# Optimization experiments

Hardware: AMD Instinct MI355X
Metric: run time of the kernel (lower is better)

Reference implementation:

```python
import jax, jax.numpy as jnp
import numpy as np

N_NODES = 50000
N_EDGES = 800000
N_GRAPHS = 1024
NODE_IN = 128
HID = 300
DEPTH = 5
READOUT = 1024


def setup_inputs() -> dict:
    key = jax.random.key(0)
    ks = jax.random.split(key, 12)
    x = jax.random.normal(ks[0], (N_NODES, NODE_IN), dtype=jnp.float32)
    edge_index = jax.random.randint(ks[1], (2, N_EDGES), 0, N_NODES, dtype=jnp.int32)
    batch = jnp.sort(jax.random.randint(ks[2], (N_NODES,), 0, N_GRAPHS, dtype=jnp.int32))
    s_in = 1.0 / np.sqrt(NODE_IN)
    s_h = 1.0 / np.sqrt(HID)
    W_proj = jax.random.normal(ks[3], (NODE_IN, HID), dtype=jnp.float32) * s_in
    b_proj = jnp.zeros((HID,), dtype=jnp.float32)
    W1 = jax.random.normal(ks[4], (DEPTH, HID, HID), dtype=jnp.float32) * s_h
    b1 = jnp.zeros((DEPTH, HID), dtype=jnp.float32)
    W2 = jax.random.normal(ks[5], (DEPTH, HID, HID), dtype=jnp.float32) * s_h
    b2 = jnp.zeros((DEPTH, HID), dtype=jnp.float32)
    W_sp = jax.random.normal(ks[6], (HID, READOUT), dtype=jnp.float32) * s_h
    b_sp = jnp.zeros((READOUT,), dtype=jnp.float32)
    prelu_a = jnp.full((1,), 0.25, dtype=jnp.float32)  # nn.PReLU default
    return {"x": x, "edge_index": edge_index, "batch": batch,
            "W_proj": W_proj, "b_proj": b_proj, "W1": W1, "b1": b1,
            "W2": W2, "b2": b2, "W_sp": W_sp, "b_sp": b_sp, "prelu_a": prelu_a}


def reference(x, edge_index, batch, W_proj, b_proj, W1, b1, W2, b2, W_sp, b_sp, prelu_a):
    # project_node_feats: Linear + ReLU
    h = jax.nn.relu(x @ W_proj + b_proj)  # [N, HID]
    src = edge_index[0]
    dst = edge_index[1]
    for i in range(DEPTH):
        # GINConv (eps=0): out = nn(x + sum_{j in N(i)} x_j)
        agg = h + jax.ops.segment_sum(h[src], dst, num_segments=N_NODES)
        h = jax.nn.relu(agg @ W1[i] + b1[i]) @ W2[i] + b2[i]
        if i < DEPTH - 1:
            h = jax.nn.relu(h)
        # dropout is identity in eval mode
    # global_add_pool over graph ids
    pooled = jax.ops.segment_sum(h, batch, num_segments=N_GRAPHS)  # [G, HID]
    z = pooled @ W_sp + b_sp  # [G, READOUT]
    # PReLU with single shared parameter
    readout = jnp.where(z >= 0, z, prelu_a[0] * z)
    return readout
```

## Files before the change

kernel.cpp:

```cpp
#include <hip/hip_runtime.h>
#include <cstdint>

#define N_NODES 50000
#define N_EDGES 800000
#define N_GRAPHS 1024
#define NODE_IN 128
#define HID 300
#define DEPTH 5
#define READOUT 1024
#define PSTR 320
#define XSTR 384

typedef float f32x4 __attribute__((ext_vector_type(4)));
typedef short bf16x8 __attribute__((ext_vector_type(8)));
typedef unsigned short us8 __attribute__((ext_vector_type(8)));

__device__ inline unsigned short f2bf(float v) {
    unsigned u = __float_as_uint(v);
    unsigned r = u + 0x7FFFu + ((u >> 16) & 1u);
    return (unsigned short)(r >> 16);
}
__device__ inline float bf2f(unsigned short h) {
    return __uint_as_float((unsigned)h << 16);
}
__device__ inline float bflo(unsigned u) { return __uint_as_float(u << 16); }
__device__ inline float bfhi(unsigned u) { return __uint_as_float(u & 0xFFFF0000u); }
__device__ inline unsigned packbf(float a, float b) {
    return (unsigned)f2bf(a) | ((unsigned)f2bf(b) << 16);
}

__global__ void hist_kernel(const int* __restrict__ dst, int* __restrict__ cnt, int n) {
    int i = blockIdx.x * blockDim.x + threadIdx.x;
    if (i < n) atomicAdd(&cnt[dst[i]], 1);
}

__global__ __launch_bounds__(256)
void scan_block(const int* __restrict__ in, int* __restrict__ out_excl,
                int* __restrict__ bsum, int n) {
    __shared__ int buf[256];
    int i = blockIdx.x * 256 + (int)threadIdx.x;
    int v = (i < n) ? in[i] : 0;
    buf[threadIdx.x] = v;
    __syncthreads();
    for (int off = 1; off < 256; off <<= 1) {
        int t = ((int)threadIdx.x >= off) ? buf[threadIdx.x - off] : 0;
        __syncthreads();
        buf[threadIdx.x] += t;
        __syncthreads();
    }
    if (i < n) out_excl[i] = buf[threadIdx.x] - v;
    if (threadIdx.x == 255) bsum[blockIdx.x] = buf[255];
}

__global__ __launch_bounds__(256)
void scan_base(const int* __restrict__ bsum, int* __restrict__ bbase, int nb,
               int* __restrict__ total) {
    __shared__ int buf[256];
    int v = ((int)threadIdx.x < nb) ? bsum[threadIdx.x] : 0;
    buf[threadIdx.x] = v;
    __syncthreads();
    for (int off = 1; off < 256; off <<= 1) {
        int t = ((int)threadIdx.x >= off) ? buf[threadIdx.x - off] : 0;
        __syncthreads();
        buf[threadIdx.x] += t;
        __syncthreads();
    }
    if ((int)threadIdx.x < nb) bbase[threadIdx.x] = buf[threadIdx.x] - v;
    if (threadIdx.x == 255) *total = buf[255];
}

__global__ void scan_add(int* __restrict__ offs, const int* __restrict__ bbase,
                         int* __restrict__ cursor, int n) {
    int i = blockIdx.x * blockDim.x + threadIdx.x;
    if (i < n) {
        int o = offs[i] + bbase[blockIdx.x];
        offs[i] = o;
        cursor[i] = o;
    }
}

__global__ void scatter_kernel(const int* __restrict__ src, const int* __restrict__ dst,
                               int* __restrict__ cursor, int* __restrict__ csr, int n) {
    int i = blockIdx.x * blockDim.x + threadIdx.x;
    if (i < n) {
        int p = atomicAdd(&cursor[dst[i]], 1);
        csr[p] = src[i];
    }
}

__global__ __launch_bounds__(256)
void aggregate_bf16(const unsigned short* __restrict__ h, const int* __restrict__ offs,
                    const int* __restrict__ csr, unsigned short* __restrict__ out) {
    int wave = (int)((blockIdx.x * blockDim.x + threadIdx.x) >> 6);
    int lane = threadIdx.x & 63;
    if (wave >= N_NODES) return;
    float a0, a1, a2, a3, a4, a5;
    {
        const unsigned* r = (const unsigned*)(h + (size_t)wave * PSTR);
        uint2 u = *(const uint2*)&r[2 * lane];
        unsigned t = (lane < 32) ? r[128 + lane] : 0u;
        a0 = bflo(u.x); a1 = bfhi(u.x);
        a2 = bflo(u.y); a3 = bfhi(u.y);
        a4 = bflo(t);   a5 = bfhi(t);
    }
    int s = offs[wave], e = offs[wave + 1];
    int k = s;
    for (; k + 3 < e; k += 4) {
        const unsigned* r0 = (const unsigned*)(h + (size_t)csr[k] * PSTR);
        const unsigned* r1 = (const unsigned*)(h + (size_t)csr[k + 1] * PSTR);
        const unsigned* r2 = (const unsigned*)(h + (size_t)csr[k + 2] * PSTR);
        const unsigned* r3 = (const unsigned*)(h + (size_t)csr[k + 3] * PSTR);
        uint2 x0 = *(const uint2*)&r0[2 * lane];
        uint2 x1 = *(const uint2*)&r1[2 * lane];
        uint2 x2 = *(const uint2*)&r2[2 * lane];
        uint2 x3 = *(const uint2*)&r3[2 * lane];
        unsigned t0 = 0, t1 = 0, t2 = 0, t3 = 0;
        if (lane < 32) {
            t0 = r0[128 + lane]; t1 = r1[128 + lane];
            t2 = r2[128 + lane]; t3 = r3[128 + lane];
        }
        a0 += bflo(x0.x) + bflo(x1.x) + bflo(x2.x) + bflo(x3.x);
        a1 += bfhi(x0.x) + bfhi(x1.x) + bfhi(x2.x) + bfhi(x3.x);
        a2 += bflo(x0.y) + bflo(x1.y) + bflo(x2.y) + bflo(x3.y);
        a3 += bfhi(x0.y) + bfhi(x1.y) + bfhi(x2.y) + bfhi(x3.y);
        a4 += bflo(t0) + bflo(t1) + bflo(t2) + bflo(t3);
        a5 += bfhi(t0) + bfhi(t1) + bfhi(t2) + bfhi(t3);
    }
    for (; k < e; ++k) {
        const unsigned* r = (const unsigned*)(h + (size_t)csr[k] * PSTR);
        uint2 u = *(const uint2*)&r[2 * lane];
        unsigned t = (lane < 32) ? r[128 + lane] : 0u;
        a0 += bflo(u.x); a1 += bfhi(u.x);
        a2 += bflo(u.y); a3 += bfhi(u.y);
        a4 += bflo(t);   a5 += bfhi(t);
    }
    unsigned* o = (unsigned*)(out + (size_t)wave * PSTR);
    uint2 w; w.x = packbf(a0, a1); w.y = packbf(a2, a3);
    *(uint2*)&o[2 * lane] = w;
    if (lane < 32) o[128 + lane] = (lane < 22) ? packbf(a4, a5) : 0u;
}

__global__ __launch_bounds__(256)
void split_weight_t(const float* __restrict__ W, int K, int N, int KP,
                    unsigned short* __restrict__ H, unsigned short* __restrict__ L) {
    __shared__ float tile[32][33];
    int n0 = blockIdx.x * 32, k0 = blockIdx.y * 32;
    int tx = threadIdx.x & 31, ty = threadIdx.x >> 5;
#pragma unroll
    for (int r = 0; r < 4; ++r) {
        int k = k0 + ty + r * 8, n = n0 + tx;
        tile[ty + r * 8][tx] = (k < K && n < N) ? W[(size_t)k * N + n] : 0.f;
    }
    __syncthreads();
#pragma unroll
    for (int r = 0; r < 4; ++r) {
        int n = n0 + ty + r * 8, k = k0 + tx;
        float v = tile[tx][ty + r * 8];
        unsigned short hb = f2bf(v);
        H[(size_t)n * KP + k] = hb;
        L[(size_t)n * KP + k] = f2bf(v - bf2f(hb));
    }
}

__global__ __launch_bounds__(256)
void split_wproj(const float* __restrict__ W, unsigned short* __restrict__ Bp) {
    __shared__ float tile[32][33];
    int n0 = blockIdx.x * 32, k0 = blockIdx.y * 32;
    int tx = threadIdx.x & 31, ty = threadIdx.x >> 5;
#pragma unroll
    for (int r = 0; r < 4; ++r) {
        int k = k0 + ty + r * 8, n = n0 + tx;
        tile[ty + r * 8][tx] = (k < NODE_IN && n < HID) ? W[(size_t)k * HID + n] : 0.f;
    }
    __syncthreads();
#pragma unroll
    for (int r = 0; r < 4; ++r) {
        int n = n0 + ty + r * 8, k = k0 + tx;
        float v = tile[tx][ty + r * 8];
        unsigned short hb = f2bf(v);
        unsigned short lb = f2bf(v - bf2f(hb));
        Bp[(size_t)n * XSTR + k] = hb;
        Bp[(size_t)n * XSTR + 128 + k] = hb;
        Bp[(size_t)n * XSTR + 256 + k] = lb;
    }
}

__global__ void split_x(const float* __restrict__ x, unsigned short* __restrict__ xs) {
    int i = blockIdx.x * blockDim.x + threadIdx.x;
    if (i >= N_NODES * 64) return;
    int row = i >> 6, c = i & 63;
    float2 v = *(const float2*)&x[(size_t)row * NODE_IN + 2 * c];
    unsigned short h0 = f2bf(v.x), h1 = f2bf(v.y);
    unsigned short l0 = f2bf(v.x - bf2f(h0)), l1 = f2bf(v.y - bf2f(h1));
    unsigned hp = (unsigned)h0 | ((unsigned)h1 << 16);
    unsigned lp = (unsigned)l0 | ((unsigned)l1 << 16);
    unsigned* o = (unsigned*)(xs + (size_t)row * XSTR);
    o[c] = hp;
    o[64 + c] = lp;
    o[128 + c] = hp;
}

#define BSWZ(r, c) ((c) ^ (((r) >> 1) & 3))
__global__ __launch_bounds__(512)
void gin_mlp(const unsigned short* __restrict__ Ap, int M,
             const unsigned short* __restrict__ B1H, const unsigned short* __restrict__ B1L,
             const float* __restrict__ b1,
             const unsigned short* __restrict__ B2H, const unsigned short* __restrict__ B2L,
             const float* __restrict__ b2,
             unsigned short* __restrict__ Op, int act2) {
    __shared__ __align__(16) unsigned short At[128 * 320];
    __shared__ __align__(16) unsigned short Bs[2 * 10240];

    const int tid = threadIdx.x;
    const int bm = blockIdx.x * 128;
    const int wid = tid >> 6, lane = tid & 63;
    const int wm = wid >> 2, wn = wid & 3;
    const int lr = lane & 15, lk = lane >> 4;

    float b1v[5], b2v[5];
#pragma unroll
    for (int n = 0; n < 5; ++n) {
        int col = wn * 80 + n * 16 + lr;
        b1v[n] = (col < HID) ? b1[col] : 0.f;
        b2v[n] = (col < HID) ? b2[col] : 0.f;
    }

#pragma unroll
    for (int i = 0; i < 10; ++i) {
        int g = i * 512 + tid;
        int row = g / 40, c = g - row * 40;
        int grow = bm + row; if (grow >= M) grow = M - 1;
        us8 v = *(const us8*)&Ap[(size_t)grow * PSTR + c * 8];
        *(us8*)&At[row * 320 + (c ^ (row & 7)) * 8] = v;
    }

    const int q = tid;
    size_t bofs[5]; int bldso[5]; bool bpl[5];
#pragma unroll
    for (int i = 0; i < 5; ++i) {
        int qq = i * 512 + q;
        bool pl = qq >= 1280;
        int q2 = qq - (pl ? 1280 : 0);
        int r = q2 >> 2, c = q2 & 3;
        bpl[i] = pl;
        bofs[i] = (size_t)r * 320 + c * 8;
        bldso[i] = (pl ? 10240 : 0) + r * 32 + BSWZ(r, c) * 8;
    }

    f32x4 acc[4][5];
    us8 vB[5];

    auto LOADB = [&](const unsigned short* BH, const unsigned short* BL, int t) {
        int k0 = t * 32;
#pragma unroll
        for (int i = 0; i < 5; ++i) {
            const unsigned short* base = bpl[i] ? BL : BH;
            vB[i] = *(const us8*)&base[bofs[i] + k0];
        }
    };
    auto RUN = [&](const unsigned short* BH, const unsigned short* BL) {
        for (int t = 0; t < 10; ++t) {
            __syncthreads();
#pragma unroll
            for (int i = 0; i < 5; ++i) *(us8*)&Bs[bldso[i]] = vB[i];
            if (t < 9) LOADB(BH, BL, t + 1);
            __syncthreads();
            bf16x8 aS[4];
#pragma unroll
            for (int m = 0; m < 4; ++m) {
                int row = wm * 64 + m * 16 + lr;
                int c = t * 4 + lk;
                aS[m] = *(const bf16x8*)&At[row * 320 + (c ^ (row & 7)) * 8];
            }
#pragma unroll
            for (int n = 0; n < 5; ++n) {
                int rb = wn * 80 + n * 16 + lr;
                int sc = rb * 32 + BSWZ(rb, lk) * 8;
                bf16x8 bh = *(const bf16x8*)&Bs[sc];
                bf16x8 bl = *(const bf16x8*)&Bs[10240 + sc];
#pragma unroll
                for (int m = 0; m < 4; ++m) {
                    acc[m][n] = __builtin_amdgcn_mfma_f32_16x16x32_bf16(aS[m], bh, acc[m][n], 0, 0, 0);
                    acc[m][n] = __builtin_amdgcn_mfma_f32_16x16x32_bf16(aS[m], bl, acc[m][n], 0, 0, 0);
                }
            }
        }
    };

#pragma unroll
    for (int m = 0; m < 4; ++m)
#pragma unroll
        for (int n = 0; n < 5; ++n) acc[m][n] = (f32x4)0.f;
    LOADB(B1H, B1L, 0);
    RUN(B1H, B1L);

    LOADB(B2H, B2L, 0);

    __syncthreads();
#pragma unroll
    for (int n = 0; n < 5; ++n) {
        int col = wn * 80 + n * 16 + lr;
        int cc = col >> 3, cp = col & 7;
        float bv = b1v[n];
        bool vc = col < HID;
#pragma unroll
        for (int m = 0; m < 4; ++m) {
#pragma unroll
            for (int p = 0; p < 4; ++p) {
                int row = wm * 64 + m * 16 + lk * 4 + p;
                float v = vc ? fmaxf(acc[m][n][p] + bv, 0.f) : 0.f;
                At[row * 320 + ((cc ^ (row & 7)) * 8) + cp] = f2bf(v);
            }
        }
    }

#pragma unroll
    for (int m = 0; m < 4; ++m)
#pragma unroll
        for (int n = 0; n < 5; ++n) acc[m][n] = (f32x4)0.f;
    RUN(B2H, B2L);

    __syncthreads();
#pragma unroll
    for (int n = 0; n < 5; ++n) {
        int col = wn * 80 + n * 16 + lr;
        int cc = col >> 3, cp = col & 7;
        float bv = b2v[n];
        bool vc = col < HID;
#pragma unroll
        for (int m = 0; m < 4; ++m) {
#pragma unroll
            for (int p = 0; p < 4; ++p) {
                int row = wm * 64 + m * 16 + lk * 4 + p;
                float v = vc ? (acc[m][n][p] + bv) : 0.f;
                if (act2) v = fmaxf(v, 0.f);
                At[row * 320 + ((cc ^ (row & 7)) * 8) + cp] = f2bf(v);
            }
        }
    }
    __syncthreads();
#pragma unroll
    for (int i = 0; i < 10; ++i) {
        int g = i * 512 + tid;
        int row = g / 40, c = g - row * 40;
        int grow = bm + row;
        if (grow < M)
            *(us8*)&Op[(size_t)grow * PSTR + c * 8] =
                *(const us8*)&At[row * 320 + (c ^ (row & 7)) * 8];
    }
}

template<int NPL>
__global__ __launch_bounds__(512)
void gemm_plane4(const unsigned short* __restrict__ Ap, int astr, int M, int KP,
                 const unsigned short* __restrict__ BH, const unsigned short* __restrict__ BL,
                 const float* __restrict__ bias, unsigned short* __restrict__ Op, int act) {
    constexpr int BITER = (NPL * 1280 + 511) / 512;
    __shared__ __align__(16) unsigned short As[2][256 * 40];
    __shared__ __align__(16) unsigned short Bs[2][NPL * 10240];

    const int tid = threadIdx.x;
    const int bm = blockIdx.x * 256;
    const int wid = tid >> 6, lane = tid & 63;
    const int wm = wid >> 2, wn = wid & 3;
    const int lr = lane & 15, lk = lane >> 4;
    const int arow = tid >> 1, ach = (tid & 1) * 2;
    int agr = bm + arow; if (agr >= M) agr = M - 1;
    const unsigned short* aSrc = Ap + (size_t)agr * astr + ach * 8;

    const unsigned short* bsrc[BITER];
    int bldso[BITER];
    bool bval[BITER];
#pragma unroll
    for (int i = 0; i < BITER; ++i) {
        int qq = i * 512 + tid;
        bval[i] = qq < NPL * 1280;
        int p = (NPL == 2 && qq >= 1280) ? 1 : 0;
        int q2 = qq - p * 1280;
        int r = q2 >> 2, c = q2 & 3;
        const unsigned short* base = p ? BL : BH;
        bsrc[i] = base + (size_t)r * KP + c * 8;
        bldso[i] = p * 10240 + r * 32 + BSWZ(r, c) * 8;
    }

    f32x4 acc[8][5];
#pragma unroll
    for (int m = 0; m < 8; ++m)
#pragma unroll
        for (int n = 0; n < 5; ++n) acc[m][n] = (f32x4)0.f;

    us8 vA0, vA1, vB[BITER];
    auto LOADS = [&](int t) {
        int k0 = t * 32;
        vA0 = *(const us8*)&aSrc[k0];
        vA1 = *(const us8*)&aSrc[k0 + 8];
#pragma unroll
        for (int i = 0; i < BITER; ++i)
            if (bval[i]) vB[i] = *(const us8*)&bsrc[i][k0];
    };
    auto WRITE = [&](int b) {
        *(us8*)&As[b][arow * 40 + ach * 8] = vA0;
        *(us8*)&As[b][arow * 40 + ach * 8 + 8] = vA1;
#pragma unroll
        for (int i = 0; i < BITER; ++i)
            if (bval[i]) *(us8*)&Bs[b][bldso[i]] = vB[i];
    };

    const int nt = KP / 32;
    LOADS(0);
    WRITE(0);
    int buf = 0;
    for (int t = 0; t < nt; ++t) {
        bool more = (t + 1 < nt);
        if (more) LOADS(t + 1);
        __syncthreads();
        bf16x8 aS[8];
#pragma unroll
        for (int m = 0; m < 8; ++m)
            aS[m] = *(const bf16x8*)&As[buf][(wm * 128 + m * 16 + lr) * 40 + lk * 8];
#pragma unroll
        for (int n = 0; n < 5; ++n) {
            int rb = wn * 80 + n * 16 + lr;
            int sc = rb * 32 + BSWZ(rb, lk) * 8;
            bf16x8 bh = *(const bf16x8*)&Bs[buf][sc];
#pragma unroll
            for (int m = 0; m < 8; ++m)
                acc[m][n] = __builtin_amdgcn_mfma_f32_16x16x32_bf16(aS[m], bh, acc[m][n], 0, 0, 0);
            if (NPL == 2) {
                bf16x8 bl = *(const bf16x8*)&Bs[buf][10240 + sc];
#pragma unroll
                for (int m = 0; m < 8; ++m)
                    acc[m][n] = __builtin_amdgcn_mfma_f32_16x16x32_bf16(aS[m], bl, acc[m][n], 0, 0, 0);
            }
        }
        if (more) WRITE(buf ^ 1);
        buf ^= 1;
    }
#pragma unroll
    for (int n = 0; n < 5; ++n) {
        int col = wn * 80 + n * 16 + lr;
        bool vc = col < HID;
        float bv = vc ? bias[col] : 0.f;
#pragma unroll
        for (int m = 0; m < 8; ++m) {
            int rbase = bm + wm * 128 + m * 16 + lk * 4;
#pragma unroll
            for (int p = 0; p < 4; ++p) {
                int row = rbase + p;
                if (row >= M) continue;
                float v = vc ? (acc[m][n][p] + bv) : 0.f;
                if (act == 1) v = fmaxf(v, 0.f);
                Op[(size_t)row * PSTR + col] = f2bf(v);
            }
        }
    }
}

__global__ __launch_bounds__(256)
void gemm_f32A(const float* __restrict__ A, int lda, int M, int K, int KP,
               const unsigned short* __restrict__ BH, const unsigned short* __restrict__ BL, int KPB,
               const float* __restrict__ bias, int N,
               float* __restrict__ C, int ldc, int act, const float* __restrict__ prelu) {
    __shared__ __align__(16) unsigned short AsH[64 * 40];
    __shared__ __align__(16) unsigned short AsL[64 * 40];
    __shared__ __align__(16) unsigned short BsH[320 * 40];
    __shared__ __align__(16) unsigned short BsL[320 * 40];

    const int tid = threadIdx.x;
    const int bm = blockIdx.y * 64;
    const int bn = blockIdx.x * 320;
    const int wid = tid >> 6, lane = tid & 63;
    const int lr = lane & 15, lk = lane >> 4;
    const int ar = tid >> 2, ac = tid & 3;

    f32x4 acc[4][5];
#pragma unroll
    for (int m = 0; m < 4; ++m)
#pragma unroll
        for (int n = 0; n < 5; ++n) acc[m][n] = (f32x4)0.f;

    for (int k0 = 0; k0 < KP; k0 += 32) {
        {
            int gm = bm + ar;
            int k = k0 + ac * 8;
            float v[8];
#pragma unroll
            for (int j = 0; j < 8; ++j) v[j] = 0.f;
            if (gm < M) {
                if (k + 7 < K) {
                    float4 p0 = *(const float4*)&A[(size_t)gm * lda + k];
                    float4 p1 = *(const float4*)&A[(size_t)gm * lda + k + 4];
                    v[0] = p0.x; v[1] = p0.y; v[2] = p0.z; v[3] = p0.w;
                    v[4] = p1.x; v[5] = p1.y; v[6] = p1.z; v[7] = p1.w;
                } else {
#pragma unroll
                    for (int j = 0; j < 8; ++j)
                        if (k + j < K) v[j] = A[(size_t)gm * lda + k + j];
                }
            }
            us8 h, l;
#pragma unroll
            for (int j = 0; j < 8; ++j) {
                unsigned short hb = f2bf(v[j]);
                h[j] = hb;
                l[j] = f2bf(v[j] - bf2f(hb));
            }
            *(us8*)&AsH[ar * 40 + ac * 8] = h;
            *(us8*)&AsL[ar * 40 + ac * 8] = l;
        }
#pragma unroll
        for (int p = 0; p < 5; ++p) {
            int r = ar + p * 64;
            size_t gb = (size_t)(bn + r) * KPB + k0 + ac * 8;
            *(us8*)&BsH[r * 40 + ac * 8] = *(const us8*)&BH[gb];
            *(us8*)&BsL[r * 40 + ac * 8] = *(const us8*)&BL[gb];
        }
        __syncthreads();
        bf16x8 aH[4], aL[4];
#pragma unroll
        for (int m = 0; m < 4; ++m) {
            aH[m] = *(const bf16x8*)&AsH[(m * 16 + lr) * 40 + lk * 8];
            aL[m] = *(const bf16x8*)&AsL[(m * 16 + lr) * 40 + lk * 8];
        }
#pragma unroll
        for (int n = 0; n < 5; ++n) {
            int r = wid * 80 + n * 16 + lr;
            bf16x8 bh = *(const bf16x8*)&BsH[r * 40 + lk * 8];
            bf16x8 bl = *(const bf16x8*)&BsL[r * 40 + lk * 8];
#pragma unroll
            for (int m = 0; m < 4; ++m) {
                acc[m][n] = __builtin_amdgcn_mfma_f32_16x16x32_bf16(aH[m], bh, acc[m][n], 0, 0, 0);
                acc[m][n] = __builtin_amdgcn_mfma_f32_16x16x32_bf16(aH[m], bl, acc[m][n], 0, 0, 0);
                acc[m][n] = __builtin_amdgcn_mfma_f32_16x16x32_bf16(aL[m], bh, acc[m][n], 0, 0, 0);
            }
        }
        __syncthreads();
    }
    float slope = (act == 2) ? prelu[0] : 0.f;
#pragma unroll
    for (int n = 0; n < 5; ++n) {
        int col = bn + wid * 80 + n * 16 + lr;
        bool vc = col < N;
        float bv = vc ? bias[col] : 0.f;
#pragma unroll
        for (int m = 0; m < 4; ++m) {
            int rbase = bm + m * 16 + lk * 4;
#pragma unroll
            for (int p = 0; p < 4; ++p) {
                int row = rbase + p;
                if (row >= M) continue;
                float v = vc ? (acc[m][n][p] + bv) : 0.f;
                if (act == 1) v = fmaxf(v, 0.f);
                else if (act == 2) v = (v >= 0.f) ? v : slope * v;
                if (vc) C[(size_t)row * ldc + col] = v;
            }
        }
    }
}

__global__ __launch_bounds__(64)
void pool_seg(const unsigned short* __restrict__ h, const int* __restrict__ goffs,
              float* __restrict__ pooled) {
    int g = blockIdx.x;
    int lane = threadIdx.x;
    int s = goffs[g], e = goffs[g + 1];
    float a0 = 0.f, a1 = 0.f, a2 = 0.f, a3 = 0.f, a4 = 0.f, a5 = 0.f;
    for (int node = s; node < e; ++node) {
        const unsigned* r = (const unsigned*)(h + (size_t)node * PSTR);
        uint2 u = *(const uint2*)&r[2 * lane];
        unsigned t = (lane < 32) ? r[128 + lane] : 0u;
        a0 += bflo(u.x); a1 += bfhi(u.x);
        a2 += bflo(u.y); a3 += bfhi(u.y);
        a4 += bflo(t);   a5 += bfhi(t);
    }
    float* pr = pooled + (size_t)g * PSTR;
    *(float4*)&pr[4 * lane] = make_float4(a0, a1, a2, a3);
    if (lane < 32) *(float2*)&pr[256 + 2 * lane] = make_float2(a4, a5);
}

extern "C" void kernel_launch(void* const* d_in, const int* in_sizes, int n_in,
                              void* d_out, int out_size, void* d_ws, size_t ws_size,
                              hipStream_t stream) {
    const float* x      = (const float*)d_in[0];
    const int*   eidx   = (const int*)d_in[1];
    const int*   batch  = (const int*)d_in[2];
    const float* W_proj = (const float*)d_in[3];
    const float* b_proj = (const float*)d_in[4];
    const float* W1     = (const float*)d_in[5];
    const float* b1     = (const float*)d_in[6];
    const float* W2     = (const float*)d_in[7];
    const float* b2     = (const float*)d_in[8];
    const float* W_sp   = (const float*)d_in[9];
    const float* b_sp   = (const float*)d_in[10];
    const float* prelu  = (const float*)d_in[11];

    const int* src = eidx;
    const int* dst = eidx + N_EDGES;

    const size_t PLANE  = (size_t)N_NODES * PSTR + 64;
    const size_t XPLANE = (size_t)N_NODES * XSTR + 64;
    const int LAYER_SZ = 320 * 320;
    const int SP_SZ    = 1280 * 320;
    const int BP_SZ    = 320 * XSTR;
    const int NB  = (N_NODES + 255) / 256;
    const int NBG = (N_GRAPHS + 255) / 256;

    unsigned short* hplane = (unsigned short*)d_ws;
    unsigned short* aggp   = hplane + PLANE;
    unsigned short* xs     = aggp;
    float* pooled = (float*)(aggp + XPLANE);
    unsigned short* w1H   = (unsigned short*)(pooled + (size_t)N_GRAPHS * PSTR + 16);
    unsigned short* w1L   = w1H + 5 * (size_t)LAYER_SZ;
    unsigned short* w2H   = w1L + 5 * (size_t)LAYER_SZ;
    unsigned short* w2L   = w2H + 5 * (size_t)LAYER_SZ;
    unsigned short* spH   = w2L + 5 * (size_t)LAYER_SZ;
    unsigned short* spL   = spH + SP_SZ;
    unsigned short* Bp    = spL + SP_SZ;
    int* cnt    = (int*)(((uintptr_t)(Bp + BP_SZ) + 15) & ~(uintptr_t)15);
    int* bsum   = cnt + N_NODES;
    int* bbase  = bsum + 256;
    int* offs   = bbase + 256;
    int* cursor = offs + N_NODES + 1;
    int* csr    = cursor + N_NODES;
    int* gcnt   = csr + N_EDGES;
    int* gsum   = gcnt + N_GRAPHS;
    int* gbase  = gsum + 256;
    int* goffs  = gbase + 256;
    int* gcur   = goffs + N_GRAPHS + 1;
    size_t needed = (size_t)((uintptr_t)(gcur + N_GRAPHS) - (uintptr_t)d_ws);
    if (ws_size < needed) return;

    split_wproj<<<dim3(10, 4), 256, 0, stream>>>(W_proj, Bp);
    for (int i = 0; i < DEPTH; ++i) {
        split_weight_t<<<dim3(10, 10), 256, 0, stream>>>(W1 + (size_t)i * HID * HID, HID, HID, 320,
                                                         w1H + (size_t)i * LAYER_SZ, w1L + (size_t)i * LAYER_SZ);
        split_weight_t<<<dim3(10, 10), 256, 0, stream>>>(W2 + (size_t)i * HID * HID, HID, HID, 320,
                                                         w2H + (size_t)i * LAYER_SZ, w2L + (size_t)i * LAYER_SZ);
    }
    split_weight_t<<<dim3(40, 10), 256, 0, stream>>>(W_sp, HID, READOUT, 320, spH, spL);

    split_x<<<(N_NODES * 64 + 255) / 256, 256, 0, stream>>>(x, xs);

    hipMemsetAsync(cnt, 0, N_NODES * sizeof(int), stream);
    hipMemsetAsync(gcnt, 0, N_GRAPHS * sizeof(int), stream);
    hist_kernel<<<(N_EDGES + 255) / 256, 256, 0, stream>>>(dst, cnt, N_EDGES);
    scan_block<<<NB, 256, 0, stream>>>(cnt, offs, bsum, N_NODES);
    scan_base<<<1, 256, 0, stream>>>(bsum, bbase, NB, offs + N_NODES);
    scan_add<<<NB, 256, 0, stream>>>(offs, bbase, cursor, N_NODES);
    scatter_kernel<<<(N_EDGES + 255) / 256, 256, 0, stream>>>(src, dst, cursor, csr, N_EDGES);

    hist_kernel<<<(N_NODES + 255) / 256, 256, 0, stream>>>(batch, gcnt, N_NODES);
    scan_block<<<NBG, 256, 0, stream>>>(gcnt, goffs, gsum, N_GRAPHS);
    scan_base<<<1, 256, 0, stream>>>(gsum, gbase, NBG, goffs + N_GRAPHS);
    scan_add<<<NBG, 256, 0, stream>>>(goffs, gbase, gcur, N_GRAPHS);

    gemm_plane4<1><<<(N_NODES + 255) / 256, 512, 0, stream>>>(
        xs, XSTR, N_NODES, XSTR, Bp, nullptr, b_proj, hplane, 1);

    const int GBM = (N_NODES + 127) / 128;
    for (int i = 0; i < DEPTH; ++i) {
        aggregate_bf16<<<(N_NODES * 64 + 255) / 256, 256, 0, stream>>>(hplane, offs, csr, aggp);
        gin_mlp<<<GBM, 512, 0, stream>>>(
            aggp, N_NODES,
            w1H + (size_t)i * LAYER_SZ, w1L + (size_t)i * LAYER_SZ, b1 + (size_t)i * HID,
            w2H + (size_t)i * LAYER_SZ, w2L + (size_t)i * LAYER_SZ, b2 + (size_t)i * HID,
            hplane, (i < DEPTH - 1) ? 1 : 0);
    }

    pool_seg<<<N_GRAPHS, 64, 0, stream>>>(hplane, goffs, pooled);

    gemm_f32A<<<dim3(4, (N_GRAPHS + 63) / 64), 256, 0, stream>>>(
        pooled, PSTR, N_GRAPHS, HID, 320, spH, spL, 320,
        b_sp, READOUT, (float*)d_out, READOUT, 2, prelu);
}
```

Before: 980.5 us.

## Fuse neighbor aggregation into GIN MLP kernel and merge setup launches

```diff
diff --git a/kernel.cpp b/kernel.cpp
--- a/kernel.cpp
+++ b/kernel.cpp
@@ -29,16 +29,23 @@
     return (unsigned)f2bf(a) | ((unsigned)f2bf(b) << 16);
 }
 
-__global__ void hist_kernel(const int* __restrict__ dst, int* __restrict__ cnt, int n) {
+__global__ void hist2(const int* __restrict__ dst, int* __restrict__ cnt,
+                      const int* __restrict__ batch, int* __restrict__ gcnt) {
     int i = blockIdx.x * blockDim.x + threadIdx.x;
-    if (i < n) atomicAdd(&cnt[dst[i]], 1);
+    if (i < N_EDGES) atomicAdd(&cnt[dst[i]], 1);
+    else if (i < N_EDGES + N_NODES) atomicAdd(&gcnt[batch[i - N_EDGES]], 1);
 }
 
 __global__ __launch_bounds__(256)
-void scan_block(const int* __restrict__ in, int* __restrict__ out_excl,
-                int* __restrict__ bsum, int n) {
+void scan_block2(const int* __restrict__ cnt, int* __restrict__ offs, int* __restrict__ bsum,
+                 const int* __restrict__ gcnt, int* __restrict__ goffs, int* __restrict__ gsum,
+                 int nbn) {
     __shared__ int buf[256];
-    int i = blockIdx.x * 256 + (int)threadIdx.x;
+    int b = blockIdx.x;
+    const int* in; int* out; int* bs; int n; int bi;
+    if (b < nbn) { in = cnt; out = offs; bs = bsum; n = N_NODES; bi = b; }
+    else { in = gcnt; out = goffs; bs = gsum; n = N_GRAPHS; bi = b - nbn; }
+    int i = bi * 256 + (int)threadIdx.x;
     int v = (i < n) ? in[i] : 0;
     buf[threadIdx.x] = v;
     __syncthreads();
@@ -48,15 +55,18 @@
         buf[threadIdx.x] += t;
         __syncthreads();
     }
-    if (i < n) out_excl[i] = buf[threadIdx.x] - v;
-    if (threadIdx.x == 255) bsum[blockIdx.x] = buf[255];
+    if (i < n) out[i] = buf[threadIdx.x] - v;
+    if (threadIdx.x == 255) bs[bi] = buf[255];
 }
 
 __global__ __launch_bounds__(256)
-void scan_base(const int* __restrict__ bsum, int* __restrict__ bbase, int nb,
-               int* __restrict__ total) {
+void scan_base2(const int* __restrict__ bsum, int* __restrict__ bbase, int nbn, int* __restrict__ tot_n,
+                const int* __restrict__ gsum, int* __restrict__ gbase, int nbg, int* __restrict__ tot_g) {
     __shared__ int buf[256];
-    int v = ((int)threadIdx.x < nb) ? bsum[threadIdx.x] : 0;
+    const int* bs; int* bb; int nb; int* tot;
+    if (blockIdx.x == 0) { bs = bsum; bb = bbase; nb = nbn; tot = tot_n; }
+    else { bs = gsum; bb = gbase; nb = nbg; tot = tot_g; }
+    int v = ((int)threadIdx.x < nb) ? bs[threadIdx.x] : 0;
     buf[threadIdx.x] = v;
     __syncthreads();
     for (int off = 1; off < 256; off <<= 1) {
@@ -65,17 +75,25 @@
         buf[threadIdx.x] += t;
         __syncthreads();
     }
-    if ((int)threadIdx.x < nb) bbase[threadIdx.x] = buf[threadIdx.x] - v;
-    if (threadIdx.x == 255) *total = buf[255];
-}
-
-__global__ void scan_add(int* __restrict__ offs, const int* __restrict__ bbase,
-                         int* __restrict__ cursor, int n) {
-    int i = blockIdx.x * blockDim.x + threadIdx.x;
-    if (i < n) {
-        int o = offs[i] + bbase[blockIdx.x];
-        offs[i] = o;
-        cursor[i] = o;
+    if ((int)threadIdx.x < nb) bb[threadIdx.x] = buf[threadIdx.x] - v;
+    if (threadIdx.x == 255) *tot = buf[255];
+}
+
+__global__ void scan_add2(int* __restrict__ offs, const int* __restrict__ bbase,
+                          int* __restrict__ cursor,
+                          int* __restrict__ goffs, const int* __restrict__ gbase, int nbn) {
+    int b = blockIdx.x;
+    if (b < nbn) {
+        int i = b * 256 + (int)threadIdx.x;
+        if (i < N_NODES) {
+            int o = offs[i] + bbase[b];
+            offs[i] = o;
+            cursor[i] = o;
+        }
+    } else {
+        int bi = b - nbn;
+        int i = bi * 256 + (int)threadIdx.x;
+        if (i < N_GRAPHS) goffs[i] += gbase[bi];
     }
 }
 
@@ -89,88 +107,36 @@
 }
 
 __global__ __launch_bounds__(256)
-void aggregate_bf16(const unsigned short* __restrict__ h, const int* __restrict__ offs,
-                    const int* __restrict__ csr, unsigned short* __restrict__ out) {
-    int wave = (int)((blockIdx.x * blockDim.x + threadIdx.x) >> 6);
-    int lane = threadIdx.x & 63;
-    if (wave >= N_NODES) return;
-    float a0, a1, a2, a3, a4, a5;
-    {
-        const unsigned* r = (const unsigned*)(h + (size_t)wave * PSTR);
-        uint2 u = *(const uint2*)&r[2 * lane];
-        unsigned t = (lane < 32) ? r[128 + lane] : 0u;
-        a0 = bflo(u.x); a1 = bfhi(u.x);
-        a2 = bflo(u.y); a3 = bfhi(u.y);
-        a4 = bflo(t);   a5 = bfhi(t);
-    }
-    int s = offs[wave], e = offs[wave + 1];
-    int k = s;
-    for (; k + 3 < e; k += 4) {
-        const unsigned* r0 = (const unsigned*)(h + (size_t)csr[k] * PSTR);
-        const unsigned* r1 = (const unsigned*)(h + (size_t)csr[k + 1] * PSTR);
-        const unsigned* r2 = (const unsigned*)(h + (size_t)csr[k + 2] * PSTR);
-        const unsigned* r3 = (const unsigned*)(h + (size_t)csr[k + 3] * PSTR);
-        uint2 x0 = *(const uint2*)&r0[2 * lane];
-        uint2 x1 = *(const uint2*)&r1[2 * lane];
-        uint2 x2 = *(const uint2*)&r2[2 * lane];
-        uint2 x3 = *(const uint2*)&r3[2 * lane];
-        unsigned t0 = 0, t1 = 0, t2 = 0, t3 = 0;
-        if (lane < 32) {
-            t0 = r0[128 + lane]; t1 = r1[128 + lane];
-            t2 = r2[128 + lane]; t3 = r3[128 + lane];
-        }
-        a0 += bflo(x0.x) + bflo(x1.x) + bflo(x2.x) + bflo(x3.x);
-        a1 += bfhi(x0.x) + bfhi(x1.x) + bfhi(x2.x) + bfhi(x3.x);
-        a2 += bflo(x0.y) + bflo(x1.y) + bflo(x2.y) + bflo(x3.y);
-        a3 += bfhi(x0.y) + bfhi(x1.y) + bfhi(x2.y) + bfhi(x3.y);
-        a4 += bflo(t0) + bflo(t1) + bflo(t2) + bflo(t3);
-        a5 += bfhi(t0) + bfhi(t1) + bfhi(t2) + bfhi(t3);
-    }
-    for (; k < e; ++k) {
-        const unsigned* r = (const unsigned*)(h + (size_t)csr[k] * PSTR);
-        uint2 u = *(const uint2*)&r[2 * lane];
-        unsigned t = (lane < 32) ? r[128 + lane] : 0u;
-        a0 += bflo(u.x); a1 += bfhi(u.x);
-        a2 += bflo(u.y); a3 += bfhi(u.y);
-        a4 += bflo(t);   a5 += bfhi(t);
-    }
-    unsigned* o = (unsigned*)(out + (size_t)wave * PSTR);
-    uint2 w; w.x = packbf(a0, a1); w.y = packbf(a2, a3);
-    *(uint2*)&o[2 * lane] = w;
-    if (lane < 32) o[128 + lane] = (lane < 22) ? packbf(a4, a5) : 0u;
-}
-
-__global__ __launch_bounds__(256)
-void split_weight_t(const float* __restrict__ W, int K, int N, int KP,
-                    unsigned short* __restrict__ H, unsigned short* __restrict__ L) {
+void split_all(const float* __restrict__ W1, const float* __restrict__ W2,
+               const float* __restrict__ Wsp, const float* __restrict__ Wproj,
+               unsigned short* __restrict__ w1H, unsigned short* __restrict__ w1L,
+               unsigned short* __restrict__ w2H, unsigned short* __restrict__ w2L,
+               unsigned short* __restrict__ spH, unsigned short* __restrict__ spL,
+               unsigned short* __restrict__ Bp) {
     __shared__ float tile[32][33];
+    const int LAYER_SZ = 320 * 320;
+    int z = blockIdx.z;
+    const float* W; unsigned short* H = nullptr; unsigned short* L = nullptr;
+    int K, N, KP;
+    if (z < 10) {
+        if (blockIdx.x >= 10) return;
+        int l = z % 5;
+        W = (z < 5 ? W1 : W2) + (size_t)l * HID * HID;
+        H = (z < 5 ? w1H : w2H) + (size_t)l * LAYER_SZ;
+        L = (z < 5 ? w1L : w2L) + (size_t)l * LAYER_SZ;
+        K = HID; N = HID; KP = 320;
+    } else if (z == 10) {
+        W = Wsp; H = spH; L = spL; K = HID; N = READOUT; KP = 320;
+    } else {
+        if (blockIdx.x >= 10 || blockIdx.y >= 4) return;
+        W = Wproj; K = NODE_IN; N = HID; KP = XSTR;
+    }
     int n0 = blockIdx.x * 32, k0 = blockIdx.y * 32;
     int tx = threadIdx.x & 31, ty = threadIdx.x >> 5;
 #pragma unroll
     for (int r = 0; r < 4; ++r) {
         int k = k0 + ty + r * 8, n = n0 + tx;
         tile[ty + r * 8][tx] = (k < K && n < N) ? W[(size_t)k * N + n] : 0.f;
-    }
-    __syncthreads();
-#pragma unroll
-    for (int r = 0; r < 4; ++r) {
-        int n = n0 + ty + r * 8, k = k0 + tx;
-        float v = tile[tx][ty + r * 8];
-        unsigned short hb = f2bf(v);
-        H[(size_t)n * KP + k] = hb;
-        L[(size_t)n * KP + k] = f2bf(v - bf2f(hb));
-    }
-}
-
-__global__ __launch_bounds__(256)
-void split_wproj(const float* __restrict__ W, unsigned short* __restrict__ Bp) {
-    __shared__ float tile[32][33];
-    int n0 = blockIdx.x * 32, k0 = blockIdx.y * 32;
-    int tx = threadIdx.x & 31, ty = threadIdx.x >> 5;
-#pragma unroll
-    for (int r = 0; r < 4; ++r) {
-        int k = k0 + ty + r * 8, n = n0 + tx;
-        tile[ty + r * 8][tx] = (k < NODE_IN && n < HID) ? W[(size_t)k * HID + n] : 0.f;
     }
     __syncthreads();
 #pragma unroll
@@ -179,9 +145,14 @@
         float v = tile[tx][ty + r * 8];
         unsigned short hb = f2bf(v);
         unsigned short lb = f2bf(v - bf2f(hb));
-        Bp[(size_t)n * XSTR + k] = hb;
-        Bp[(size_t)n * XSTR + 128 + k] = hb;
-        Bp[(size_t)n * XSTR + 256 + k] = lb;
+        if (z < 11) {
+            H[(size_t)n * KP + k] = hb;
+            L[(size_t)n * KP + k] = lb;
+        } else {
+            Bp[(size_t)n * XSTR + k] = hb;
+            Bp[(size_t)n * XSTR + 128 + k] = hb;
+            Bp[(size_t)n * XSTR + 256 + k] = lb;
+        }
     }
 }
 
@@ -201,13 +172,15 @@
 }
 
 #define BSWZ(r, c) ((c) ^ (((r) >> 1) & 3))
+
 __global__ __launch_bounds__(512)
-void gin_mlp(const unsigned short* __restrict__ Ap, int M,
-             const unsigned short* __restrict__ B1H, const unsigned short* __restrict__ B1L,
-             const float* __restrict__ b1,
-             const unsigned short* __restrict__ B2H, const unsigned short* __restrict__ B2L,
-             const float* __restrict__ b2,
-             unsigned short* __restrict__ Op, int act2) {
+void gin_layer(const unsigned short* __restrict__ h, const int* __restrict__ offs,
+               const int* __restrict__ csr, int M,
+               const unsigned short* __restrict__ B1H, const unsigned short* __restrict__ B1L,
+               const float* __restrict__ b1,
+               const unsigned short* __restrict__ B2H, const unsigned short* __restrict__ B2L,
+               const float* __restrict__ b2,
+               unsigned short* __restrict__ Op, int act2) {
     __shared__ __align__(16) unsigned short At[128 * 320];
     __shared__ __align__(16) unsigned short Bs[2 * 10240];
 
@@ -225,20 +198,10 @@
         b2v[n] = (col < HID) ? b2[col] : 0.f;
     }
 
-#pragma unroll
-    for (int i = 0; i < 10; ++i) {
-        int g = i * 512 + tid;
-        int row = g / 40, c = g - row * 40;
-        int grow = bm + row; if (grow >= M) grow = M - 1;
-        us8 v = *(const us8*)&Ap[(size_t)grow * PSTR + c * 8];
-        *(us8*)&At[row * 320 + (c ^ (row & 7)) * 8] = v;
-    }
-
-    const int q = tid;
     size_t bofs[5]; int bldso[5]; bool bpl[5];
 #pragma unroll
     for (int i = 0; i < 5; ++i) {
-        int qq = i * 512 + q;
+        int qq = i * 512 + tid;
         bool pl = qq >= 1280;
         int q2 = qq - (pl ? 1280 : 0);
         int r = q2 >> 2, c = q2 & 3;
@@ -247,9 +210,7 @@
         bldso[i] = (pl ? 10240 : 0) + r * 32 + BSWZ(r, c) * 8;
     }
 
-    f32x4 acc[4][5];
     us8 vB[5];
-
     auto LOADB = [&](const unsigned short* BH, const unsigned short* BL, int t) {
         int k0 = t * 32;
 #pragma unroll
@@ -258,6 +219,65 @@
             vB[i] = *(const us8*)&base[bofs[i] + k0];
         }
     };
+
+    LOADB(B1H, B1L, 0);
+
+    unsigned* At_dw = (unsigned*)At;
+    for (int j = 0; j < 16; ++j) {
+        int row = wid * 16 + j;
+        int g = bm + row;
+        float a0 = 0.f, a1 = 0.f, a2 = 0.f, a3 = 0.f, a4 = 0.f, a5 = 0.f;
+        if (g < M) {
+            const unsigned* rr = (const unsigned*)(h + (size_t)g * PSTR);
+            uint2 u = *(const uint2*)&rr[2 * lane];
+            unsigned t = (lane < 32) ? rr[128 + lane] : 0u;
+            a0 = bflo(u.x); a1 = bfhi(u.x);
+            a2 = bflo(u.y); a3 = bfhi(u.y);
+            a4 = bflo(t);   a5 = bfhi(t);
+            int s = offs[g], e = offs[g + 1];
+            int k = s;
+            for (; k + 3 < e; k += 4) {
+                const unsigned* r0 = (const unsigned*)(h + (size_t)csr[k] * PSTR);
+                const unsigned* r1 = (const unsigned*)(h + (size_t)csr[k + 1] * PSTR);
+                const unsigned* r2 = (const unsigned*)(h + (size_t)csr[k + 2] * PSTR);
+                const unsigned* r3 = (const unsigned*)(h + (size_t)csr[k + 3] * PSTR);
+                uint2 x0 = *(const uint2*)&r0[2 * lane];
+                uint2 x1 = *(const uint2*)&r1[2 * lane];
+                uint2 x2 = *(const uint2*)&r2[2 * lane];
+                uint2 x3 = *(const uint2*)&r3[2 * lane];
+                unsigned t0 = 0, t1 = 0, t2 = 0, t3 = 0;
+                if (lane < 32) {
+                    t0 = r0[128 + lane]; t1 = r1[128 + lane];
+                    t2 = r2[128 + lane]; t3 = r3[128 + lane];
+                }
+                a0 += bflo(x0.x) + bflo(x1.x) + bflo(x2.x) + bflo(x3.x);
+                a1 += bfhi(x0.x) + bfhi(x1.x) + bfhi(x2.x) + bfhi(x3.x);
+                a2 += bflo(x0.y) + bflo(x1.y) + bflo(x2.y) + bflo(x3.y);
+                a3 += bfhi(x0.y) + bfhi(x1.y) + bfhi(x2.y) + bfhi(x3.y);
+                a4 += bflo(t0) + bflo(t1) + bflo(t2) + bflo(t3);
+                a5 += bfhi(t0) + bfhi(t1) + bfhi(t2) + bfhi(t3);
+            }
+            for (; k < e; ++k) {
+                const unsigned* r4 = (const unsigned*)(h + (size_t)csr[k] * PSTR);
+                uint2 u4 = *(const uint2*)&r4[2 * lane];
+                unsigned t4 = (lane < 32) ? r4[128 + lane] : 0u;
+                a0 += bflo(u4.x); a1 += bfhi(u4.x);
+                a2 += bflo(u4.y); a3 += bfhi(u4.y);
+                a4 += bflo(t4);   a5 += bfhi(t4);
+            }
+        }
+        int rb = row * 160;
+        int c0 = ((lane >> 1) ^ (row & 7)) * 4 + (lane & 1) * 2;
+        uint2 wv; wv.x = packbf(a0, a1); wv.y = packbf(a2, a3);
+        *(uint2*)&At_dw[rb + c0] = wv;
+        if (lane < 32) {
+            int cc = (32 + (lane >> 2)) ^ (row & 7);
+            At_dw[rb + cc * 4 + (lane & 3)] = (lane < 22) ? packbf(a4, a5) : 0u;
+        }
+    }
+
+    f32x4 acc[4][5];
+
     auto RUN = [&](const unsigned short* BH, const unsigned short* BL) {
         for (int t = 0; t < 10; ++t) {
             __syncthreads();
@@ -274,8 +294,8 @@
             }
 #pragma unroll
             for (int n = 0; n < 5; ++n) {
-                int rb = wn * 80 + n * 16 + lr;
-                int sc = rb * 32 + BSWZ(rb, lk) * 8;
+                int rb2 = wn * 80 + n * 16 + lr;
+                int sc = rb2 * 32 + BSWZ(rb2, lk) * 8;
                 bf16x8 bh = *(const bf16x8*)&Bs[sc];
                 bf16x8 bl = *(const bf16x8*)&Bs[10240 + sc];
 #pragma unroll
@@ -291,7 +311,6 @@
     for (int m = 0; m < 4; ++m)
 #pragma unroll
         for (int n = 0; n < 5; ++n) acc[m][n] = (f32x4)0.f;
-    LOADB(B1H, B1L, 0);
     RUN(B1H, B1L);
 
     LOADB(B2H, B2L, 0);
@@ -605,69 +624,58 @@
     const int NB  = (N_NODES + 255) / 256;
     const int NBG = (N_GRAPHS + 255) / 256;
 
-    unsigned short* hplane = (unsigned short*)d_ws;
-    unsigned short* aggp   = hplane + PLANE;
-    unsigned short* xs     = aggp;
-    float* pooled = (float*)(aggp + XPLANE);
-    unsigned short* w1H   = (unsigned short*)(pooled + (size_t)N_GRAPHS * PSTR + 16);
-    unsigned short* w1L   = w1H + 5 * (size_t)LAYER_SZ;
-    unsigned short* w2H   = w1L + 5 * (size_t)LAYER_SZ;
-    unsigned short* w2L   = w2H + 5 * (size_t)LAYER_SZ;
-    unsigned short* spH   = w2L + 5 * (size_t)LAYER_SZ;
-    unsigned short* spL   = spH + SP_SZ;
-    unsigned short* Bp    = spL + SP_SZ;
+    unsigned short* hA  = (unsigned short*)d_ws;
+    unsigned short* hBx = hA + PLANE;
+    unsigned short* xs  = hBx;
+    float* pooled = (float*)(hBx + XPLANE);
+    unsigned short* w1H = (unsigned short*)(pooled + (size_t)N_GRAPHS * PSTR + 16);
+    unsigned short* w1L = w1H + 5 * (size_t)LAYER_SZ;
+    unsigned short* w2H = w1L + 5 * (size_t)LAYER_SZ;
+    unsigned short* w2L = w2H + 5 * (size_t)LAYER_SZ;
+    unsigned short* spH = w2L + 5 * (size_t)LAYER_SZ;
+    unsigned short* spL = spH + SP_SZ;
+    unsigned short* Bp  = spL + SP_SZ;
     int* cnt    = (int*)(((uintptr_t)(Bp + BP_SZ) + 15) & ~(uintptr_t)15);
-    int* bsum   = cnt + N_NODES;
+    int* gcnt   = cnt + N_NODES;
+    int* bsum   = gcnt + N_GRAPHS;
     int* bbase  = bsum + 256;
-    int* offs   = bbase + 256;
-    int* cursor = offs + N_NODES + 1;
+    int* gsum   = bbase + 256;
+    int* gbase  = gsum + 256;
+    int* offs   = gbase + 256;
+    int* goffs  = offs + N_NODES + 1;
+    int* cursor = goffs + N_GRAPHS + 1;
     int* csr    = cursor + N_NODES;
-    int* gcnt   = csr + N_EDGES;
-    int* gsum   = gcnt + N_GRAPHS;
-    int* gbase  = gsum + 256;
-    int* goffs  = gbase + 256;
-    int* gcur   = goffs + N_GRAPHS + 1;
-    size_t needed = (size_t)((uintptr_t)(gcur + N_GRAPHS) - (uintptr_t)d_ws);
+    size_t needed = (size_t)((uintptr_t)(csr + N_EDGES) - (uintptr_t)d_ws);
     if (ws_size < needed) return;
 
-    split_wproj<<<dim3(10, 4), 256, 0, stream>>>(W_proj, Bp);
+    split_all<<<dim3(40, 10, 12), 256, 0, stream>>>(W1, W2, W_sp, W_proj,
+                                                    w1H, w1L, w2H, w2L, spH, spL, Bp);
+    split_x<<<(N_NODES * 64 + 255) / 256, 256, 0, stream>>>(x, xs);
+
+    hipMemsetAsync(cnt, 0, (N_NODES + N_GRAPHS) * sizeof(int), stream);
+    hist2<<<(N_EDGES + N_NODES + 255) / 256, 256, 0, stream>>>(dst, cnt, batch, gcnt);
+    scan_block2<<<NB + NBG, 256, 0, stream>>>(cnt, offs, bsum, gcnt, goffs, gsum, NB);
+    scan_base2<<<2, 256, 0, stream>>>(bsum, bbase, NB, offs + N_NODES,
+                                      gsum, gbase, NBG, goffs + N_GRAPHS);
+    scan_add2<<<NB + NBG, 256, 0, stream>>>(offs, bbase, cursor, goffs, gbase, NB);
+    scatter_kernel<<<(N_EDGES + 255) / 256, 256, 0, stream>>>(src, dst, cursor, csr, N_EDGES);
+
+    gemm_plane4<1><<<(N_NODES + 255) / 256, 512, 0, stream>>>(
+        xs, XSTR, N_NODES, XSTR, Bp, nullptr, b_proj, hA, 1);
+
+    const int GBM = (N_NODES + 127) / 128;
+    unsigned short* cur = hA;
+    unsigned short* nxt = hBx;
     for (int i = 0; i < DEPTH; ++i) {
-        split_weight_t<<<dim3(10, 10), 256, 0, stream>>>(W1 + (size_t)i * HID * HID, HID, HID, 320,
-                                                         w1H + (size_t)i * LAYER_SZ, w1L + (size_t)i * LAYER_SZ);
-        split_weight_t<<<dim3(10, 10), 256, 0, stream>>>(W2 + (size_t)i * HID * HID, HID, HID, 320,
-                                                         w2H + (size_t)i * LAYER_SZ, w2L + (size_t)i * LAYER_SZ);
-    }
-    split_weight_t<<<dim3(40, 10), 256, 0, stream>>>(W_sp, HID, READOUT, 320, spH, spL);
-
-    split_x<<<(N_NODES * 64 + 255) / 256, 256, 0, stream>>>(x, xs);
-
-    hipMemsetAsync(cnt, 0, N_NODES * sizeof(int), stream);
-    hipMemsetAsync(gcnt, 0, N_GRAPHS * sizeof(int), stream);
-    hist_kernel<<<(N_EDGES + 255) / 256, 256, 0, stream>>>(dst, cnt, N_EDGES);
-    scan_block<<<NB, 256, 0, stream>>>(cnt, offs, bsum, N_NODES);
-    scan_base<<<1, 256, 0, stream>>>(bsum, bbase, NB, offs + N_NODES);
-    scan_add<<<NB, 256, 0, stream>>>(offs, bbase, cursor, N_NODES);
-    scatter_kernel<<<(N_EDGES + 255) / 256, 256, 0, stream>>>(src, dst, cursor, csr, N_EDGES);
-
-    hist_kernel<<<(N_NODES + 255) / 256, 256, 0, stream>>>(batch, gcnt, N_NODES);
-    scan_block<<<NBG, 256, 0, stream>>>(gcnt, goffs, gsum, N_GRAPHS);
-    scan_base<<<1, 256, 0, stream>>>(gsum, gbase, NBG, goffs + N_GRAPHS);
-    scan_add<<<NBG, 256, 0, stream>>>(goffs, gbase, gcur, N_GRAPHS);
-
-    gemm_plane4<1><<<(N_NODES + 255) / 256, 512, 0, stream>>>(
-        xs, XSTR, N_NODES, XSTR, Bp, nullptr, b_proj, hplane, 1);
-
-    const int GBM = (N_NODES + 127) / 128;
-    for (int i = 0; i < DEPTH; ++i) {
-        aggregate_bf16<<<(N_NODES * 64 + 255) / 256, 256, 0, stream>>>(hplane, offs, csr, aggp);
-        gin_mlp<<<GBM, 512, 0, stream>>>(
-            aggp, N_NODES,
+        gin_layer<<<GBM, 512, 0, stream>>>(
+            cur, offs, csr, N_NODES,
             w1H + (size_t)i * LAYER_SZ, w1L + (size_t)i * LAYER_SZ, b1 + (size_t)i * HID,
             w2H + (size_t)i * LAYER_SZ, w2L + (size_t)i * LAYER_SZ, b2 + (size_t)i * HID,
-            hplane, (i < DEPTH - 1) ? 1 : 0);
-    }
-
-    pool_seg<<<N_GRAPHS, 64, 0, stream>>>(hplane, goffs, pooled);
+            nxt, (i < DEPTH - 1) ? 1 : 0);
+        unsigned short* t = cur; cur = nxt; nxt = t;
+    }
+
+    pool_seg<<<N_GRAPHS, 64, 0, stream>>>(cur, goffs, pooled);
 
     gemm_f32A<<<dim3(4, (N_GRAPHS + 63) / 64), 256, 0, stream>>>(
         pooled, PSTR, N_GRAPHS, HID, 320, spH, spL, 320,
```

Measured after the change: 1.273 ms. 29.8% more time.
